# Optimization experiments

Hardware: AMD Instinct MI355X
Metric: run time of the kernel (lower is better)

Reference implementation:

```python
import jax, jax.numpy as jnp
import numpy as np

B, LQ, LK, D = 32, 1024, 1024, 256

def setup_inputs() -> dict:
    key = jax.random.key(0)
    ks = jax.random.split(key, 7)
    return {
        "raw_query": jax.random.normal(ks[0], (B, LQ, D), dtype=jnp.float32),
        "raw_key": jax.random.normal(ks[1], (B, LK, D), dtype=jnp.float32),
        "raw_value": jax.random.normal(ks[2], (B, LK, D), dtype=jnp.float32),
        "value_mask": jax.random.randint(ks[3], (B, LQ), 0, 2, dtype=jnp.int32),
        "WQ": jax.random.normal(ks[4], (D, D), dtype=jnp.float32) * 0.05,
        "WK": jax.random.normal(ks[5], (D, D), dtype=jnp.float32) * 0.05,
        "WV": jax.random.normal(ks[6], (D, D), dtype=jnp.float32) * 0.05,
    }

def reference(raw_query, raw_key, raw_value, value_mask, WQ, WK, WV):
    # Projections: [B, L, D] @ [D, D]
    Q = raw_query @ WQ
    K = raw_key @ WK
    V = raw_value @ WV
    # Scores: [B, LQ, LK] (use_scale=False -> no 1/sqrt(d_k))
    att = jnp.einsum("bqd,bkd->bqk", Q, K)
    # Mask expanded on axis=2 -> zeroes entire query rows of scores (faithful to tf.where+zeros_like)
    att = jnp.where(value_mask[:, :, None] > 0, att, jnp.zeros((), dtype=att.dtype))
    att = jax.nn.softmax(att, axis=-1)
    # Output: [B, LQ, D]
    return jnp.einsum("bqk,bkd->bqd", att, V)
```

## Files before the change

kernel.cpp:

```cpp
#include <hip/hip_runtime.h>
#include <hip/hip_bf16.h>
#include <math.h>

#define B_ 32
#define L_ 1024
#define D_ 256

typedef _Float16 half8 __attribute__((ext_vector_type(8)));
typedef __fp16   fp16x2 __attribute__((ext_vector_type(2)));
typedef short    s16x8 __attribute__((ext_vector_type(8)));
typedef float    f32x4 __attribute__((ext_vector_type(4)));

typedef __attribute__((address_space(3))) unsigned int lds_u32;
typedef __attribute__((address_space(1))) unsigned int gbl_u32;

__device__ __forceinline__ void gl_lds16(const void* g, void* l) {
    __builtin_amdgcn_global_load_lds((gbl_u32*)g, (lds_u32*)l, 16, 0, 0);
}

__device__ __forceinline__ unsigned short f2bf(float x) {
    unsigned u = __float_as_uint(x);
    u += 0x7FFFu + ((u >> 16) & 1u);
    return (unsigned short)(u >> 16);
}

__device__ __forceinline__ unsigned short f2h(float x) {
    _Float16 h = (_Float16)x;
    unsigned short u;
    __builtin_memcpy(&u, &h, 2);
    return u;
}

__device__ __forceinline__ unsigned pkrtz(float a, float b) {
    fp16x2 v = __builtin_amdgcn_cvt_pkrtz(a, b);
    unsigned u;
    __builtin_memcpy(&u, &v, 4);
    return u;
}

#define WAITVL(N) asm volatile("s_waitcnt vmcnt(" #N ") lgkmcnt(0)" ::: "memory")
#define WAITV(N)  asm volatile("s_waitcnt vmcnt(" #N ")" ::: "memory")
#define BARRIER()  do { __builtin_amdgcn_s_barrier(); __builtin_amdgcn_sched_barrier(0); } while (0)

__global__ __launch_bounds__(256) void wprep_kernel(
    const float* __restrict__ W0, const float* __restrict__ W1,
    const float* __restrict__ W2, unsigned short* __restrict__ Wt)
{
    const int z = blockIdx.z;
    const float* __restrict__ W = (z == 0) ? W0 : (z == 1) ? W1 : W2;
    __shared__ unsigned short T[64][72];
    const int k0 = blockIdx.x << 6, n0 = blockIdx.y << 6;
    const int t = threadIdx.x;
    const int r = t >> 2, c0 = (t & 3) << 4;
    #pragma unroll
    for (int j = 0; j < 16; j += 4) {
        float4 w4 = *(const float4*)(W + (size_t)(k0 + r) * 256 + n0 + c0 + j);
        T[c0 + j + 0][r] = f2h(w4.x);
        T[c0 + j + 1][r] = f2h(w4.y);
        T[c0 + j + 2][r] = f2h(w4.z);
        T[c0 + j + 3][r] = f2h(w4.w);
    }
    __syncthreads();
    const int n = t >> 2, kc = (t & 3) << 4;
    unsigned short* dst = Wt + ((size_t)z << 16) + (size_t)(n0 + n) * 256 + k0 + kc;
    *(uint4*)(dst + 0) = *(const uint4*)&T[n][kc + 0];
    *(uint4*)(dst + 8) = *(const uint4*)&T[n][kc + 8];
}

__global__ __launch_bounds__(1024, 4) void proj_mfma_kernel(
    const float* __restrict__ A0, const float* __restrict__ A1,
    const float* __restrict__ A2, const unsigned short* __restrict__ Wt,
    unsigned short* __restrict__ Qh, unsigned short* __restrict__ Kh,
    unsigned short* __restrict__ Vt)
{
    __shared__ __align__(16) unsigned char SMEMRAW[131072];
    float*          Asm = (float*)SMEMRAW;
    unsigned short* Bsm = (unsigned short*)(SMEMRAW + 65536);

    const int fblk = blockIdx.x;
    const int xt = fblk & 255;
    const int z  = fblk >> 8;
    const int bm = xt << 7;

    const float* __restrict__ A = (z == 0) ? A0 : (z == 1) ? A1 : A2;
    const int t = threadIdx.x, lane = t & 63, w = t >> 6;
    const int wm = (w >> 2) << 5, wn = (w & 3) << 6;

    const float* __restrict__ Ag = A + (size_t)bm * 256;
    const unsigned short* __restrict__ Bg = Wt + ((size_t)z << 16);

    f32x4 acc[2][4];
    const f32x4 z4 = {0.f, 0.f, 0.f, 0.f};
    #pragma unroll
    for (int mi = 0; mi < 2; ++mi)
        #pragma unroll
        for (int ni = 0; ni < 4; ++ni) acc[mi][ni] = z4;

    auto stageA = [&](int buf, int it) {
        #pragma unroll
        for (int i = 0; i < 2; ++i) {
            int o = (i << 10) + t;
            int r = o >> 4, c = o & 15;
            int cs = (c & 8) | ((c & 7) ^ (r & 7));
            gl_lds16(Ag + (size_t)r * 256 + (it << 6) + (cs << 2),
                     &Asm[(buf << 13) + (o << 2)]);
        }
    };
    auto stageB = [&](int buf, int it) {
        #pragma unroll
        for (int i = 0; i < 2; ++i) {
            int o = (i << 10) + t;
            int r = o >> 3, c = o & 7;
            int cs = c ^ (r & 7);
            gl_lds16(Bg + (size_t)r * 256 + (it << 6) + (cs << 3),
                     &Bsm[(buf << 14) + (o << 3)]);
        }
    };
    auto compute = [&](int buf) {
        #pragma unroll
        for (int kc = 0; kc < 2; ++kc) {
            half8 af[2], bfr[4];
            #pragma unroll
            for (int mi = 0; mi < 2; ++mi) {
                int m  = wm + (mi << 4) + (lane & 15);
                int g2 = (lane >> 4) << 1;
                int cs0 = (kc << 3) | ( g2      ^ (m & 7));
                int cs1 = (kc << 3) | ((g2 | 1) ^ (m & 7));
                float4 lo = *(const float4*)&Asm[(buf << 13) + (m << 6) + (cs0 << 2)];
                float4 hi = *(const float4*)&Asm[(buf << 13) + (m << 6) + (cs1 << 2)];
                unsigned hh[4];
                hh[0] = pkrtz(lo.x, lo.y); hh[1] = pkrtz(lo.z, lo.w);
                hh[2] = pkrtz(hi.x, hi.y); hh[3] = pkrtz(hi.z, hi.w);
                __builtin_memcpy(&af[mi], hh, 16);
            }
            #pragma unroll
            for (int ni = 0; ni < 4; ++ni) {
                int n = wn + (ni << 4) + (lane & 15);
                int cs = ((kc << 2) + (lane >> 4)) ^ (n & 7);
                bfr[ni] = *(const half8*)&Bsm[(buf << 14) + (n << 6) + (cs << 3)];
            }
            #pragma unroll
            for (int mi = 0; mi < 2; ++mi)
                #pragma unroll
                for (int ni = 0; ni < 4; ++ni)
                    acc[mi][ni] = __builtin_amdgcn_mfma_f32_16x16x32_f16(
                        af[mi], bfr[ni], acc[mi][ni], 0, 0, 0);
        }
    };

    stageA(0, 0); stageB(0, 0);
    WAITVL(0); BARRIER();

    stageA(1, 1); stageB(1, 1);
    WAITVL(4); BARRIER();
    compute(0);
    BARRIER();
    stageA(0, 2); stageB(0, 2);
    WAITVL(4); BARRIER();
    compute(1);
    BARRIER();
    stageA(1, 3); stageB(1, 3);
    WAITVL(4); BARRIER();
    compute(0);
    BARRIER();
    WAITVL(0); BARRIER();
    compute(1);

    if (z < 2) {
        unsigned short* __restrict__ C = (z == 0) ? Qh : Kh;
        __syncthreads();
        unsigned short (*Cs)[264] = (unsigned short(*)[264])SMEMRAW;
        #pragma unroll
        for (int mi = 0; mi < 2; ++mi) {
            int q0l = wm + (mi << 4) + ((lane >> 4) << 2);
            #pragma unroll
            for (int ni = 0; ni < 4; ++ni) {
                int cl = wn + (ni << 4) + (lane & 15);
                #pragma unroll
                for (int r = 0; r < 4; ++r)
                    Cs[q0l + r][cl] = f2h(acc[mi][ni][r]);
            }
        }
        __syncthreads();
        #pragma unroll
        for (int i = 0; i < 4; ++i) {
            int o = (i << 10) + t;
            int r = o >> 5, c = o & 31;
            *(uint4*)(C + (size_t)(bm + r) * 256 + (c << 3)) =
                *(const uint4*)&Cs[r][c << 3];
        }
    } else {
        unsigned short (*Tt)[136] = (unsigned short(*)[136])SMEMRAW;
        const int bb = bm >> 10, kin = bm & 1023;
        #pragma unroll
        for (int dh = 0; dh < 2; ++dh) {
            __syncthreads();
            if (((w & 3) >> 1) == dh) {
                #pragma unroll
                for (int mi = 0; mi < 2; ++mi) {
                    int m0 = wm + (mi << 4) + ((lane >> 4) << 2);
                    #pragma unroll
                    for (int ni = 0; ni < 4; ++ni) {
                        int nl = (wn & 127) + (ni << 4) + (lane & 15);
                        #pragma unroll
                        for (int r = 0; r < 4; ++r)
                            Tt[nl][m0 + r] = f2bf(acc[mi][ni][r]);
                    }
                }
            }
            __syncthreads();
            int dr = t >> 3, cq = t & 7;
            unsigned short* dst = Vt + ((size_t)bb * 256 + (dh << 7) + dr) * 1024
                                  + kin + (cq << 4);
            *(uint4*)(dst + 0) = *(const uint4*)&Tt[dr][(cq << 4) + 0];
            *(uint4*)(dst + 8) = *(const uint4*)&Tt[dr][(cq << 4) + 8];
        }
    }
}

__global__ __launch_bounds__(1024, 4) void fused_attn_kernel(
    const unsigned short* __restrict__ Qh, const unsigned short* __restrict__ Kh,
    const unsigned short* __restrict__ Vt, const int* __restrict__ mask,
    float* __restrict__ Out)
{
    __shared__ unsigned short Ks[2][16384];
    __shared__ unsigned short Vs[2][16384];
    __shared__ unsigned short Ps[128 * 64];
    float* lredp = (float*)Ps;

    const int f  = blockIdx.x;
    const int b  = (f & 7) + ((f >> 6) << 3);
    const int q0 = ((f >> 3) & 7) << 7;
    const size_t bL = (size_t)b * L_;
    const int t = threadIdx.x, lane = t & 63, w = t >> 6;
    const int wm_s = (w >> 1) << 4, wn_s = (w & 1) << 5;
    const int wm_v = (w >> 2) << 5, wn_v = (w & 3) << 6;

    const unsigned short* __restrict__ Kb = Kh + (bL << 8);
    const unsigned short* __restrict__ Vb = Vt + (bL << 8);

    auto stageK = [&](int buf, int kt) {
        #pragma unroll
        for (int i = 0; i < 1; ++i) { }
        #pragma unroll
        for (int i = 0; i < 2; ++i) {
            int o = (i << 10) + t;
            int r = o >> 5, c = o & 31;
            int cs = (c & 24) | ((c & 7) ^ (r & 7));
            gl_lds16(Kb + (size_t)((kt << 6) + r) * 256 + (cs << 3), &Ks[buf][o << 3]);
        }
    };
    auto stageV = [&](int buf, int kt) {
        #pragma unroll
        for (int i = 0; i < 2; ++i) {
            int o = (i << 10) + t;
            int d = o >> 3, c = o & 7;
            int cs = c ^ (d & 7);
            gl_lds16(Vb + ((size_t)d << 10) + (kt << 6) + (cs << 3), &Vs[buf][o << 3]);
        }
    };

    half8 qf[8];
    {
        int m = wm_s + (lane & 15);
        const unsigned short* qp = Qh + ((bL + q0 + m) << 8) + ((lane >> 4) << 3);
        #pragma unroll
        for (int kc = 0; kc < 8; ++kc)
            qf[kc] = *(const half8*)(qp + (kc << 5));
    }
    int mv[4];
    {
        int qrow = wm_s + ((lane >> 4) << 2);
        #pragma unroll
        for (int r = 0; r < 4; ++r) mv[r] = mask[bL + q0 + qrow + r];
    }
    stageK(0, 0);
    stageV(0, 0);

    f32x4 o_acc[2][4];
    const f32x4 z4 = {0.f, 0.f, 0.f, 0.f};
    #pragma unroll
    for (int mi = 0; mi < 2; ++mi)
        #pragma unroll
        for (int ni = 0; ni < 4; ++ni) o_acc[mi][ni] = z4;
    float lacc[4] = {};

    WAITVL(0); BARRIER();

    for (int kt = 0; kt < 16; ++kt) {
        const int cur = kt & 1;
        if (kt < 15) {
            stageK(cur ^ 1, kt + 1);
            stageV(cur ^ 1, kt + 1);
        }

        f32x4 accs[2];
        accs[0] = z4; accs[1] = z4;
        #pragma unroll
        for (int kc = 0; kc < 8; ++kc) {
            int kb = (kc >> 1) << 6, cc = ((kc & 1) << 2) + (lane >> 4);
            int n0 = wn_s + (lane & 15);
            int n1 = n0 + 16;
            half8 bf0 = *(const half8*)&Ks[cur][(n0 << 8) + kb + ((cc ^ (n0 & 7)) << 3)];
            half8 bf1 = *(const half8*)&Ks[cur][(n1 << 8) + kb + ((cc ^ (n1 & 7)) << 3)];
            accs[0] = __builtin_amdgcn_mfma_f32_16x16x32_f16(qf[kc], bf0, accs[0], 0, 0, 0);
            accs[1] = __builtin_amdgcn_mfma_f32_16x16x32_f16(qf[kc], bf1, accs[1], 0, 0, 0);
        }

        {
            int qrow = wm_s + ((lane >> 4) << 2);
            #pragma unroll
            for (int ni = 0; ni < 2; ++ni) {
                int kl = wn_s + (ni << 4) + (lane & 15);
                #pragma unroll
                for (int r = 0; r < 4; ++r) {
                    int q = qrow + r;
                    float p = mv[r] ? __expf(accs[ni][r]) : 1.0f;
                    Ps[(q << 6) + ((((kl >> 3) ^ (q & 7)) << 3)) + (kl & 7)] = f2bf(p);
                    lacc[r] += p;
                }
            }
        }
        if (kt < 15) { WAITVL(4); } else { WAITVL(0); }
        BARRIER();

        #pragma unroll
        for (int kc2 = 0; kc2 < 2; ++kc2) {
            s16x8 pa[2], vb[4];
            int cc = (kc2 << 2) + (lane >> 4);
            #pragma unroll
            for (int mi = 0; mi < 2; ++mi) {
                int m = wm_v + (mi << 4) + (lane & 15);
                pa[mi] = *(const s16x8*)&Ps[(m << 6) + ((cc ^ (m & 7)) << 3)];
            }
            #pragma unroll
            for (int ni = 0; ni < 4; ++ni) {
                int n = wn_v + (ni << 4) + (lane & 15);
                vb[ni] = *(const s16x8*)&Vs[cur][(n << 6) + ((cc ^ (n & 7)) << 3)];
            }
            #pragma unroll
            for (int mi = 0; mi < 2; ++mi)
                #pragma unroll
                for (int ni = 0; ni < 4; ++ni)
                    o_acc[mi][ni] = __builtin_amdgcn_mfma_f32_16x16x32_bf16(
                        pa[mi], vb[ni], o_acc[mi][ni], 0, 0, 0);
        }
        if (kt < 15) { WAITV(2); }
        BARRIER();
    }

    #pragma unroll
    for (int r = 0; r < 4; ++r) {
        float v = lacc[r];
        v += __shfl_xor(v, 1);
        v += __shfl_xor(v, 2);
        v += __shfl_xor(v, 4);
        v += __shfl_xor(v, 8);
        if ((lane & 15) == 0)
            lredp[((wm_s + ((lane >> 4) << 2) + r) << 1) + (w & 1)] = v;
    }
    __syncthreads();

    #pragma unroll
    for (int mi = 0; mi < 2; ++mi) {
        #pragma unroll
        for (int rr = 0; rr < 4; ++rr) {
            int q = wm_v + (mi << 4) + ((lane >> 4) << 2) + rr;
            float inv = 1.0f / (lredp[q << 1] + lredp[(q << 1) + 1]);
            #pragma unroll
            for (int ni = 0; ni < 4; ++ni) {
                int d = wn_v + (ni << 4) + (lane & 15);
                Out[((bL + q0 + q) << 8) + d] = o_acc[mi][ni][rr] * inv;
            }
        }
    }
}

extern "C" void kernel_launch(void* const* d_in, const int* in_sizes, int n_in,
                              void* d_out, int out_size, void* d_ws, size_t ws_size,
                              hipStream_t stream) {
    const float* rq = (const float*)d_in[0];
    const float* rk = (const float*)d_in[1];
    const float* rv = (const float*)d_in[2];
    const int*   vm = (const int*)d_in[3];
    const float* WQ = (const float*)d_in[4];
    const float* WK = (const float*)d_in[5];
    const float* WV = (const float*)d_in[6];
    float* out = (float*)d_out;

    char* ws = (char*)d_ws;
    unsigned short* Qh = (unsigned short*)(ws);
    unsigned short* Kh = (unsigned short*)(ws + ((size_t)16 << 20));
    unsigned short* Vt = (unsigned short*)(ws + ((size_t)32 << 20));
    unsigned short* Wt = (unsigned short*)(ws + ((size_t)48 << 20));

    dim3 wg(4, 4, 3);
    wprep_kernel<<<wg, 256, 0, stream>>>(WQ, WK, WV, Wt);

    proj_mfma_kernel<<<768, 1024, 0, stream>>>(rq, rk, rv, Wt, Qh, Kh, Vt);

    fused_attn_kernel<<<256, 1024, 0, stream>>>(Qh, Kh, Vt, vm, out);
}
```

Measured before the change: 91.77 us.

## Restructure attention kernel to 32x32 MFMA, 128-key tiles, 512 threads

The fused attention kernel now runs 8 waves of 512 threads, each computing a 32-row query tile with 32x32x16 MFMAs instead of 16x16x32. Key tiles grow from 64 to 128 keys, which halves the loop trip count. The double-buffered K/V staging is replaced by single buffers: V is loaded while QK runs, and the next K is loaded while PV runs. The aim is fewer barriers and LDS reads per MFMA and larger matrix instructions. In exchange, load latency is hidden less well and register pressure rises, with 64 accumulators per thread plus 16 Q fragments.

After: 134.7 us. 1.47x slower.

```diff
diff --git a/kernel.cpp b/kernel.cpp
--- a/kernel.cpp
+++ b/kernel.cpp
@@ -10,6 +10,7 @@
 typedef __fp16   fp16x2 __attribute__((ext_vector_type(2)));
 typedef short    s16x8 __attribute__((ext_vector_type(8)));
 typedef float    f32x4 __attribute__((ext_vector_type(4)));
+typedef float    f32x16 __attribute__((ext_vector_type(16)));
 
 typedef __attribute__((address_space(3))) unsigned int lds_u32;
 typedef __attribute__((address_space(1))) unsigned int gbl_u32;
@@ -39,7 +40,6 @@
 }
 
 #define WAITVL(N) asm volatile("s_waitcnt vmcnt(" #N ") lgkmcnt(0)" ::: "memory")
-#define WAITV(N)  asm volatile("s_waitcnt vmcnt(" #N ")" ::: "memory")
 #define BARRIER()  do { __builtin_amdgcn_s_barrier(); __builtin_amdgcn_sched_barrier(0); } while (0)
 
 __global__ __launch_bounds__(256) void wprep_kernel(
@@ -218,160 +218,145 @@
     }
 }
 
-__global__ __launch_bounds__(1024, 4) void fused_attn_kernel(
+__global__ __launch_bounds__(512, 2) void fused_attn_kernel(
     const unsigned short* __restrict__ Qh, const unsigned short* __restrict__ Kh,
     const unsigned short* __restrict__ Vt, const int* __restrict__ mask,
     float* __restrict__ Out)
 {
-    __shared__ unsigned short Ks[2][16384];
-    __shared__ unsigned short Vs[2][16384];
-    __shared__ unsigned short Ps[128 * 64];
+    __shared__ unsigned short Ks[128 * 256];
+    __shared__ unsigned short Vs[256 * 128];
+    __shared__ unsigned short Ps[128 * 128];
     float* lredp = (float*)Ps;
 
     const int f  = blockIdx.x;
     const int b  = (f & 7) + ((f >> 6) << 3);
-    const int q0 = ((f >> 3) & 7) << 7;
+    const int q0blk = ((f >> 3) & 7) << 7;
     const size_t bL = (size_t)b * L_;
     const int t = threadIdx.x, lane = t & 63, w = t >> 6;
-    const int wm_s = (w >> 1) << 4, wn_s = (w & 1) << 5;
-    const int wm_v = (w >> 2) << 5, wn_v = (w & 3) << 6;
+    const int q0w  = (w >> 1) << 5;
+    const int wn_k = (w & 1) << 6;
+    const int d0w  = (w & 1) << 7;
+    const int hi4  = (lane >> 5) << 2;
 
     const unsigned short* __restrict__ Kb = Kh + (bL << 8);
     const unsigned short* __restrict__ Vb = Vt + (bL << 8);
 
-    auto stageK = [&](int buf, int kt) {
-        #pragma unroll
-        for (int i = 0; i < 1; ++i) { }
-        #pragma unroll
-        for (int i = 0; i < 2; ++i) {
-            int o = (i << 10) + t;
+    auto stageK = [&](int kt) {
+        #pragma unroll
+        for (int i = 0; i < 8; ++i) {
+            int o = (i << 9) + t;
             int r = o >> 5, c = o & 31;
-            int cs = (c & 24) | ((c & 7) ^ (r & 7));
-            gl_lds16(Kb + (size_t)((kt << 6) + r) * 256 + (cs << 3), &Ks[buf][o << 3]);
-        }
-    };
-    auto stageV = [&](int buf, int kt) {
-        #pragma unroll
-        for (int i = 0; i < 2; ++i) {
-            int o = (i << 10) + t;
-            int d = o >> 3, c = o & 7;
-            int cs = c ^ (d & 7);
-            gl_lds16(Vb + ((size_t)d << 10) + (kt << 6) + (cs << 3), &Vs[buf][o << 3]);
-        }
-    };
-
-    half8 qf[8];
+            int cs = c ^ (r & 31);
+            gl_lds16(Kb + (size_t)((kt << 7) + r) * 256 + (cs << 3), &Ks[o << 3]);
+        }
+    };
+    auto stageV = [&](int kt) {
+        #pragma unroll
+        for (int i = 0; i < 8; ++i) {
+            int o = (i << 9) + t;
+            int d = o >> 4, c = o & 15;
+            int cs = c ^ (d & 15);
+            gl_lds16(Vb + ((size_t)d << 10) + (kt << 7) + (cs << 3), &Vs[o << 3]);
+        }
+    };
+
+    half8 qf[16];
     {
-        int m = wm_s + (lane & 15);
-        const unsigned short* qp = Qh + ((bL + q0 + m) << 8) + ((lane >> 4) << 3);
-        #pragma unroll
-        for (int kc = 0; kc < 8; ++kc)
-            qf[kc] = *(const half8*)(qp + (kc << 5));
-    }
-    int mv[4];
-    {
-        int qrow = wm_s + ((lane >> 4) << 2);
-        #pragma unroll
-        for (int r = 0; r < 4; ++r) mv[r] = mask[bL + q0 + qrow + r];
-    }
-    stageK(0, 0);
-    stageV(0, 0);
-
-    f32x4 o_acc[2][4];
-    const f32x4 z4 = {0.f, 0.f, 0.f, 0.f};
-    #pragma unroll
-    for (int mi = 0; mi < 2; ++mi)
-        #pragma unroll
-        for (int ni = 0; ni < 4; ++ni) o_acc[mi][ni] = z4;
-    float lacc[4] = {};
-
-    WAITVL(0); BARRIER();
-
-    for (int kt = 0; kt < 16; ++kt) {
-        const int cur = kt & 1;
-        if (kt < 15) {
-            stageK(cur ^ 1, kt + 1);
-            stageV(cur ^ 1, kt + 1);
-        }
-
-        f32x4 accs[2];
-        accs[0] = z4; accs[1] = z4;
-        #pragma unroll
-        for (int kc = 0; kc < 8; ++kc) {
-            int kb = (kc >> 1) << 6, cc = ((kc & 1) << 2) + (lane >> 4);
-            int n0 = wn_s + (lane & 15);
-            int n1 = n0 + 16;
-            half8 bf0 = *(const half8*)&Ks[cur][(n0 << 8) + kb + ((cc ^ (n0 & 7)) << 3)];
-            half8 bf1 = *(const half8*)&Ks[cur][(n1 << 8) + kb + ((cc ^ (n1 & 7)) << 3)];
-            accs[0] = __builtin_amdgcn_mfma_f32_16x16x32_f16(qf[kc], bf0, accs[0], 0, 0, 0);
-            accs[1] = __builtin_amdgcn_mfma_f32_16x16x32_f16(qf[kc], bf1, accs[1], 0, 0, 0);
-        }
-
-        {
-            int qrow = wm_s + ((lane >> 4) << 2);
-            #pragma unroll
-            for (int ni = 0; ni < 2; ++ni) {
-                int kl = wn_s + (ni << 4) + (lane & 15);
-                #pragma unroll
-                for (int r = 0; r < 4; ++r) {
-                    int q = qrow + r;
-                    float p = mv[r] ? __expf(accs[ni][r]) : 1.0f;
-                    Ps[(q << 6) + ((((kl >> 3) ^ (q & 7)) << 3)) + (kl & 7)] = f2bf(p);
-                    lacc[r] += p;
-                }
-            }
-        }
-        if (kt < 15) { WAITVL(4); } else { WAITVL(0); }
-        BARRIER();
-
-        #pragma unroll
-        for (int kc2 = 0; kc2 < 2; ++kc2) {
-            s16x8 pa[2], vb[4];
-            int cc = (kc2 << 2) + (lane >> 4);
-            #pragma unroll
-            for (int mi = 0; mi < 2; ++mi) {
-                int m = wm_v + (mi << 4) + (lane & 15);
-                pa[mi] = *(const s16x8*)&Ps[(m << 6) + ((cc ^ (m & 7)) << 3)];
-            }
-            #pragma unroll
-            for (int ni = 0; ni < 4; ++ni) {
-                int n = wn_v + (ni << 4) + (lane & 15);
-                vb[ni] = *(const s16x8*)&Vs[cur][(n << 6) + ((cc ^ (n & 7)) << 3)];
-            }
-            #pragma unroll
-            for (int mi = 0; mi < 2; ++mi)
-                #pragma unroll
-                for (int ni = 0; ni < 4; ++ni)
-                    o_acc[mi][ni] = __builtin_amdgcn_mfma_f32_16x16x32_bf16(
-                        pa[mi], vb[ni], o_acc[mi][ni], 0, 0, 0);
-        }
-        if (kt < 15) { WAITV(2); }
-        BARRIER();
-    }
-
-    #pragma unroll
-    for (int r = 0; r < 4; ++r) {
+        const unsigned short* qp = Qh + ((bL + q0blk + q0w + (lane & 31)) << 8)
+                                   + ((lane >> 5) << 3);
+        #pragma unroll
+        for (int st = 0; st < 16; ++st)
+            qf[st] = *(const half8*)(qp + (st << 4));
+    }
+    unsigned mvbits = 0;
+    #pragma unroll
+    for (int r = 0; r < 16; ++r) {
+        int q = q0w + (r & 3) + ((r >> 2) << 3) + hi4;
+        mvbits |= (mask[bL + q0blk + q] ? 1u : 0u) << r;
+    }
+    stageK(0);
+
+    f32x16 o_acc[4];
+    const f32x16 z16 = {0.f,0.f,0.f,0.f,0.f,0.f,0.f,0.f,0.f,0.f,0.f,0.f,0.f,0.f,0.f,0.f};
+    #pragma unroll
+    for (int di = 0; di < 4; ++di) o_acc[di] = z16;
+    float lacc[16];
+    #pragma unroll
+    for (int r = 0; r < 16; ++r) lacc[r] = 0.f;
+
+    __syncthreads();
+
+    for (int kt = 0; kt < 8; ++kt) {
+        stageV(kt);
+
+        f32x16 accs[2];
+        accs[0] = z16; accs[1] = z16;
+        #pragma unroll
+        for (int st = 0; st < 16; ++st) {
+            int ch = (st << 1) + (lane >> 5);
+            int n0 = wn_k + (lane & 31);
+            int n1 = n0 + 32;
+            half8 bf0 = *(const half8*)&Ks[(n0 << 8) + ((ch ^ (n0 & 31)) << 3)];
+            half8 bf1 = *(const half8*)&Ks[(n1 << 8) + ((ch ^ (n1 & 31)) << 3)];
+            accs[0] = __builtin_amdgcn_mfma_f32_32x32x16_f16(qf[st], bf0, accs[0], 0, 0, 0);
+            accs[1] = __builtin_amdgcn_mfma_f32_32x32x16_f16(qf[st], bf1, accs[1], 0, 0, 0);
+        }
+
+        #pragma unroll
+        for (int ns = 0; ns < 2; ++ns) {
+            int k = wn_k + (ns << 5) + (lane & 31);
+            int ch = k >> 3, klo = k & 7;
+            #pragma unroll
+            for (int r = 0; r < 16; ++r) {
+                int q = q0w + (r & 3) + ((r >> 2) << 3) + hi4;
+                float p = ((mvbits >> r) & 1) ? __expf(accs[ns][r]) : 1.0f;
+                Ps[(q << 7) + ((ch ^ (q & 15)) << 3) + klo] = f2bf(p);
+                lacc[r] += p;
+            }
+        }
+        __syncthreads();
+
+        if (kt < 7) stageK(kt + 1);
+
+        #pragma unroll
+        for (int ks = 0; ks < 8; ++ks) {
+            int ch = (ks << 1) + (lane >> 5);
+            int q = q0w + (lane & 31);
+            s16x8 pa = *(const s16x8*)&Ps[(q << 7) + ((ch ^ (q & 15)) << 3)];
+            #pragma unroll
+            for (int di = 0; di < 4; ++di) {
+                int d = d0w + (di << 5) + (lane & 31);
+                s16x8 vb = *(const s16x8*)&Vs[(d << 7) + ((ch ^ (d & 15)) << 3)];
+                o_acc[di] = __builtin_amdgcn_mfma_f32_32x32x16_bf16(
+                    pa, vb, o_acc[di], 0, 0, 0);
+            }
+        }
+        __syncthreads();
+    }
+
+    #pragma unroll
+    for (int r = 0; r < 16; ++r) {
         float v = lacc[r];
         v += __shfl_xor(v, 1);
         v += __shfl_xor(v, 2);
         v += __shfl_xor(v, 4);
         v += __shfl_xor(v, 8);
-        if ((lane & 15) == 0)
-            lredp[((wm_s + ((lane >> 4) << 2) + r) << 1) + (w & 1)] = v;
+        v += __shfl_xor(v, 16);
+        if ((lane & 31) == 0) {
+            int q = q0w + (r & 3) + ((r >> 2) << 3) + hi4;
+            lredp[(q << 1) + (w & 1)] = v;
+        }
     }
     __syncthreads();
 
     #pragma unroll
-    for (int mi = 0; mi < 2; ++mi) {
-        #pragma unroll
-        for (int rr = 0; rr < 4; ++rr) {
-            int q = wm_v + (mi << 4) + ((lane >> 4) << 2) + rr;
-            float inv = 1.0f / (lredp[q << 1] + lredp[(q << 1) + 1]);
-            #pragma unroll
-            for (int ni = 0; ni < 4; ++ni) {
-                int d = wn_v + (ni << 4) + (lane & 15);
-                Out[((bL + q0 + q) << 8) + d] = o_acc[mi][ni][rr] * inv;
-            }
+    for (int r = 0; r < 16; ++r) {
+        int q = q0w + (r & 3) + ((r >> 2) << 3) + hi4;
+        float inv = 1.0f / (lredp[q << 1] + lredp[(q << 1) + 1]);
+        #pragma unroll
+        for (int di = 0; di < 4; ++di) {
+            int d = d0w + (di << 5) + (lane & 31);
+            Out[((bL + q0blk + q) << 8) + d] = o_acc[di][r] * inv;
         }
     }
 }
@@ -399,5 +384,5 @@
 
     proj_mfma_kernel<<<768, 1024, 0, stream>>>(rq, rk, rv, Wt, Qh, Kh, Vt);
 
-    fused_attn_kernel<<<256, 1024, 0, stream>>>(Qh, Kh, Vt, vm, out);
-}
+    fused_attn_kernel<<<256, 512, 0, stream>>>(Qh, Kh, Vt, vm, out);
+}
```
